# Kernel optimization log

Hardware: AMD Instinct MI355X
Metric: run time of the kernel (lower is better)

The kernel has to match this reference:

```python
import jax, jax.numpy as jnp
import numpy as np

# dims derived from init_kwargs
B, C, T, F = 16, 2, 16, 256
TP, FP = 4, 4            # time/freq patch
MF = F // FP             # 64 freq tokens
TIC = T // TP            # 4 time tokens per chunk
S = MF * TIC             # 256 tokens per chunk
CTX = 3
LEFT = S * CTX           # 768 cached tokens
MT = TIC * (CTX + 1)     # 16 max time positions
D, H, G = 512, 8, 4      # d_model, q heads, kv groups
HD = D // H              # 64
R = H // G               # 2 q-heads per kv group
L = 4                    # layers
FFH = 4 * D
EPS = 1e-5


def _ln(x, g, b):
    m = jnp.mean(x, -1, keepdims=True)
    v = jnp.mean((x - m) ** 2, -1, keepdims=True)
    return (x - m) * jax.lax.rsqrt(v + EPS) * g + b


def setup_inputs() -> dict:
    key = jax.random.key(0)
    ks = iter(jax.random.split(key, 20))
    rn = lambda shape, s=0.05: jax.random.normal(next(ks), shape, jnp.float32) * s
    return {
        "x": rn((B, C, T, F), 1.0),
        "cache_k": rn((L, B, G, LEFT, HD), 1.0),
        "cache_v": rn((L, B, G, LEFT, HD), 1.0),
        "in_W": rn((TP * FP * C, D)), "in_b": jnp.zeros((D,)),
        "ln1_g": jnp.ones((L, D)), "ln1_b": jnp.zeros((L, D)),
        "Wq": rn((L, D, D)), "bq": jnp.zeros((L, D)),
        "Wk": rn((L, D, G * HD)), "bk": jnp.zeros((L, G * HD)),
        "Wv": rn((L, D, G * HD)), "bv": jnp.zeros((L, G * HD)),
        "Wo": rn((L, D, D)), "bo": jnp.zeros((L, D)),
        "rel_time": rn((L, 2 * MT - 1, H)), "rel_freq": rn((L, 2 * MF - 1, H)),
        "res_a": jnp.ones((L,)),
        "ln2_g": jnp.ones((L, D)), "ln2_b": jnp.zeros((L, D)),
        "W1": rn((L, D, FFH)), "b1": jnp.zeros((L, FFH)),
        "W3": rn((L, D, FFH)), "b3": jnp.zeros((L, FFH)),
        "W2": rn((L, FFH, D)), "b2": jnp.zeros((L, D)),
        "res_f": jnp.ones((L,)),
        "out_W": rn((D, TP * FP * C)), "out_b": jnp.zeros((TP * FP * C,)),
    }


def reference(x, cache_k, cache_v, in_W, in_b, ln1_g, ln1_b, Wq, bq, Wk, bk, Wv, bv,
              Wo, bo, rel_time, rel_freq, res_a, ln2_g, ln2_b, W1, b1, W3, b3, W2, b2,
              res_f, out_W, out_b):
    # patchify: (B,C,T,F) -> (B, S, TP*FP*C), token order time-major / freq inner
    h = jnp.transpose(x, (0, 2, 3, 1)).reshape(B, TIC, TP, MF, FP, C)
    h = jnp.transpose(h, (0, 1, 3, 2, 4, 5)).reshape(B, S, TP * FP * C)
    h = h @ in_W + in_b  # (B,S,D)

    # 2D relative position indices (identical each layer)
    K = LEFT + S
    q_idx = jnp.arange(S)
    k_idx = jnp.arange(K)
    qt = LEFT // MF + q_idx // MF  # query time = cache time offset + local time
    qf = q_idx % MF
    kt = k_idx // MF
    kf = k_idx % MF
    dt = qt[:, None] - kt[None, :] + (MT - 1)  # (S,K) in [0, 2*MT-2]
    df = qf[:, None] - kf[None, :] + (MF - 1)  # (S,K) in [0, 2*MF-2]
    scale = 1.0 / np.sqrt(HD).astype(np.float32)

    new_ck, new_cv = [], []
    for l in range(L):
        # --- streaming GQA attention with 2D rel-pos and KV cache ---
        xin = _ln(h, ln1_g[l], ln1_b[l])
        q = (xin @ Wq[l] + bq[l]).reshape(B, S, H, HD)
        k = (xin @ Wk[l] + bk[l]).reshape(B, S, G, HD)
        v = (xin @ Wv[l] + bv[l]).reshape(B, S, G, HD)
        k_full = jnp.concatenate([cache_k[l], jnp.transpose(k, (0, 2, 1, 3))], axis=2)  # (B,G,K,HD)
        v_full = jnp.concatenate([cache_v[l], jnp.transpose(v, (0, 2, 1, 3))], axis=2)
        new_ck.append(k_full[:, :, -LEFT:])
        new_cv.append(v_full[:, :, -LEFT:])
        # group q heads: head h -> group h // R
        scores = jnp.einsum('bsgrd,bgtd->bgrst', q.reshape(B, S, G, R, HD), k_full) * scale
        bias = rel_time[l][dt] + rel_freq[l][df]          # (S,K,H)
        bias = jnp.transpose(bias, (2, 0, 1)).reshape(G, R, S, K)
        attn = jax.nn.softmax(scores + bias[None], axis=-1)
        o = jnp.einsum('bgrst,bgtd->bsgrd', attn, v_full).reshape(B, S, D)
        o = o @ Wo[l] + bo[l]
        h = h + res_a[l] * o  # dropout/droppath identity at eval
        # --- SwiGLU FFN ---
        xin = _ln(h, ln2_g[l], ln2_b[l])
        ff = (jax.nn.silu(xin @ W1[l] + b1[l]) * (xin @ W3[l] + b3[l])) @ W2[l] + b2[l]
        h = h + res_f[l] * ff

    y = h @ out_W + out_b  # (B,S,TP*FP*C)
    # unpatchify back to (B,C,T,F)
    y = y.reshape(B, TIC, MF, TP, FP, C)
    y = jnp.transpose(y, (0, 1, 3, 2, 4, 5)).reshape(B, T, F, C)
    y = jnp.transpose(y, (0, 3, 1, 2))
    return y, jnp.stack(new_ck), jnp.stack(new_cv)
```

## Files before the change

### kernel.cpp

```cpp
#include <hip/hip_runtime.h>
#include <stdint.h>

typedef __attribute__((ext_vector_type(8))) short bf16x8;
typedef __attribute__((ext_vector_type(4))) float f32x4;

#define B_    16
#define S_    256
#define LEFT_ 768
#define KT_   1024
#define D_    512
#define H_    8
#define G_    4
#define HD_   64
#define L_    4
#define FFH_  2048
#define M_    4096

__device__ __forceinline__ unsigned short f2b(float f){
  unsigned u = __float_as_uint(f);
  u += 0x7fffu + ((u>>16)&1u);
  return (unsigned short)(u>>16);
}

__device__ __forceinline__ void gl_lds16(const unsigned short* g, void* l){
  __builtin_amdgcn_global_load_lds(
    (const __attribute__((address_space(1))) unsigned int*)g,
    (__attribute__((address_space(3))) unsigned int*)l, 16, 0, 0);
}

template<int BM, int BN, int WM, int WN, class BRowF>
__device__ __forceinline__ void mfma_core(
    const unsigned short* Abase, int lda, int m0, BRowF brow,
    int kd, char* As, char* Bs, f32x4* acc)
{
  constexpr int FR = WM/16, FC = WN/16;
  constexpr int NWC = BN/WN;
  constexpr int CA = BM/64, CB = BN/64;
  const int tid = threadIdx.x, wave = tid>>6, lane = tid&63;
  const int wr = wave / NWC, wc = wave % NWC;
  const int lr = lane>>2;
  const int swl = (lane&3) ^ ((lane>>2)&3) ^ (lane>>4);

  auto stage = [&](int buf, int k0){
    #pragma unroll
    for (int i = 0; i < CA; ++i) {
      const int chunk = wave*CA + i;
      const unsigned short* gp = Abase + (size_t)(m0 + chunk*16 + lr)*lda + k0 + swl*8;
      gl_lds16(gp, As + buf*(BM*64) + chunk*1024);
    }
    #pragma unroll
    for (int i = 0; i < CB; ++i) {
      const int chunk = wave*CB + i;
      const unsigned short* gp = brow(chunk*16 + lr) + k0 + swl*8;
      gl_lds16(gp, Bs + buf*(BN*64) + chunk*1024);
    }
  };

  stage(0, 0);
  __syncthreads();
  int cur = 0;
  for (int k0 = 0; k0 < kd; k0 += 32) {
    if (k0 + 32 < kd) stage(cur^1, k0 + 32);
    bf16x8 af[FR], bfr[FC];
    #pragma unroll
    for (int r = 0; r < FR; ++r)
      af[r] = *(const bf16x8*)(As + cur*(BM*64) + (wr*WM + r*16 + (lane&15))*64 + swl*16);
    #pragma unroll
    for (int c = 0; c < FC; ++c)
      bfr[c] = *(const bf16x8*)(Bs + cur*(BN*64) + (wc*WN + c*16 + (lane&15))*64 + swl*16);
    #pragma unroll
    for (int r = 0; r < FR; ++r)
      #pragma unroll
      for (int c = 0; c < FC; ++c)
        acc[r*FC+c] = __builtin_amdgcn_mfma_f32_16x16x32_bf16(af[r], bfr[c], acc[r*FC+c], 0, 0, 0);
    __syncthreads();
    cur ^= 1;
  }
}

__device__ __forceinline__ void tcvt_body(
    const float* __restrict__ src, unsigned short* __restrict__ dst,
    int K, int N, int ntk, int ntn, int bx)
{
  __shared__ float t[64][65];
  int kt = bx % ntk; int nt = (bx/ntk) % ntn; int l = bx/(ntk*ntn);
  src += (size_t)l*K*N; dst += (size_t)l*N*K;
  const int k0 = kt*64, n0 = nt*64;
  const int tid = threadIdx.x;
  #pragma unroll
  for (int i = 0; i < 4; ++i) {
    int kr = (tid>>4) + i*16;
    const float4 v = *(const float4*)&src[(size_t)(k0+kr)*N + n0 + (tid&15)*4];
    t[kr][(tid&15)*4+0]=v.x; t[kr][(tid&15)*4+1]=v.y;
    t[kr][(tid&15)*4+2]=v.z; t[kr][(tid&15)*4+3]=v.w;
  }
  __syncthreads();
  const int nn = tid>>2, kk = (tid&3)*16;
  unsigned w[8];
  #pragma unroll
  for (int j = 0; j < 8; ++j)
    w[j] = (unsigned)f2b(t[kk+2*j][nn]) | ((unsigned)f2b(t[kk+2*j+1][nn])<<16);
  size_t off = (size_t)(n0+nn)*K + k0 + kk;
  *(uint4*)&dst[off]     = make_uint4(w[0],w[1],w[2],w[3]);
  *(uint4*)&dst[off + 8] = make_uint4(w[4],w[5],w[6],w[7]);
}

__global__ __launch_bounds__(256) void transpose_all(
    const float* __restrict__ Wq, const float* __restrict__ Wk,
    const float* __restrict__ Wv, const float* __restrict__ Wo,
    const float* __restrict__ W1, const float* __restrict__ W3,
    const float* __restrict__ W2,
    unsigned short* __restrict__ Wqt, unsigned short* __restrict__ Wkt,
    unsigned short* __restrict__ Wvt, unsigned short* __restrict__ Wot,
    unsigned short* __restrict__ W1t, unsigned short* __restrict__ W3t,
    unsigned short* __restrict__ W2t)
{
  int bx = blockIdx.x;
  if      (bx < 256)  tcvt_body(Wq, Wqt, 512, 512, 8, 8,  bx);
  else if (bx < 384)  tcvt_body(Wk, Wkt, 512, 256, 8, 4,  bx-256);
  else if (bx < 512)  tcvt_body(Wv, Wvt, 512, 256, 8, 4,  bx-384);
  else if (bx < 768)  tcvt_body(Wo, Wot, 512, 512, 8, 8,  bx-512);
  else if (bx < 1792) tcvt_body(W1, W1t, 512, 2048, 8, 32, bx-768);
  else if (bx < 2816) tcvt_body(W3, W3t, 512, 2048, 8, 32, bx-1792);
  else                tcvt_body(W2, W2t, 2048, 512, 32, 8, bx-2816);
}

__global__ __launch_bounds__(256) void patchify_inproj(
    const float* __restrict__ x, const float* __restrict__ inW,
    const float* __restrict__ inb, float* __restrict__ h)
{
  int bs = blockIdx.x;
  int b = bs >> 8, s = bs & 255;
  int tic = s >> 6, mf = s & 63;
  __shared__ float ps[32];
  int tid = threadIdx.x;
  if (tid < 32) {
    int tp = tid >> 3, fp = (tid >> 1) & 3, c = tid & 1;
    ps[tid] = x[((size_t)(b*2 + c)*16 + tic*4 + tp)*256 + mf*4 + fp];
  }
  __syncthreads();
  #pragma unroll
  for (int rep = 0; rep < 2; ++rep) {
    int d = tid + rep*256;
    float acc = inb[d];
    #pragma unroll
    for (int i = 0; i < 32; ++i) acc += ps[i] * inW[i*D_ + d];
    h[(size_t)bs*D_ + d] = acc;
  }
}

__global__ __launch_bounds__(256) void ln_kernel(
    const float* __restrict__ in, unsigned short* __restrict__ out,
    const float* __restrict__ g, const float* __restrict__ bta)
{
  size_t row = blockIdx.x;
  const float* rp = in + row*D_;
  int tid = threadIdx.x;
  float x0 = rp[tid], x1 = rp[tid+256];
  float s = x0 + x1, sq = x0*x0 + x1*x1;
  __shared__ float red[10];
  #pragma unroll
  for (int o = 32; o > 0; o >>= 1) {
    s  += __shfl_down(s,  o, 64);
    sq += __shfl_down(sq, o, 64);
  }
  if ((tid & 63) == 0) { red[tid>>6] = s; red[4 + (tid>>6)] = sq; }
  __syncthreads();
  if (tid == 0) {
    float ts = red[0]+red[1]+red[2]+red[3];
    float tq = red[4]+red[5]+red[6]+red[7];
    float mean = ts * (1.0f/D_);
    float var  = tq * (1.0f/D_) - mean*mean;
    red[8] = mean; red[9] = 1.0f / sqrtf(var + 1e-5f);
  }
  __syncthreads();
  float mean = red[8], inv = red[9];
  unsigned short* op = out + row*D_;
  op[tid]     = f2b((x0-mean)*inv*g[tid]     + bta[tid]);
  op[tid+256] = f2b((x1-mean)*inv*g[tid+256] + bta[tid+256]);
}

__global__ __launch_bounds__(256) void qkv_ln_gemm(
    const float* __restrict__ h,
    const float* __restrict__ lng, const float* __restrict__ lnb,
    const unsigned short* __restrict__ Wqt, const unsigned short* __restrict__ Wkt,
    const unsigned short* __restrict__ Wvt,
    const float* __restrict__ bq, const float* __restrict__ bk_, const float* __restrict__ bv_,
    unsigned short* __restrict__ q_bf, unsigned short* __restrict__ kf_bf,
    unsigned short* __restrict__ vt_bf, float* __restrict__ nck, float* __restrict__ ncv)
{
  __shared__ alignas(16) char As[2][64*64];
  __shared__ alignas(16) char Bs[2][128*64];
  __shared__ float sm[64], sr[64];
  const int bx = blockIdx.x;
  const int mt = bx >> 3, nt = bx & 7;
  const int m0 = mt*64, n0 = nt*128;
  const int tid = threadIdx.x, wave = tid>>6, lane = tid&63;

  {
    const int r = tid >> 2, qd = tid & 3;
    const float* rp = h + (size_t)(m0 + r)*512 + qd*128;
    float s = 0.f, sq = 0.f;
    #pragma unroll
    for (int i = 0; i < 32; ++i) {
      float4 v = ((const float4*)rp)[i];
      s  += (v.x+v.y)+(v.z+v.w);
      sq += (v.x*v.x+v.y*v.y)+(v.z*v.z+v.w*v.w);
    }
    s += __shfl_xor(s,1,64); sq += __shfl_xor(sq,1,64);
    s += __shfl_xor(s,2,64); sq += __shfl_xor(sq,2,64);
    if (qd == 0) {
      float mean = s*(1.f/512.f);
      sm[r] = mean;
      sr[r] = rsqrtf(sq*(1.f/512.f) - mean*mean + 1e-5f);
    }
  }

  const int ar = tid >> 2, au = tid & 3;
  const int ap = au ^ (ar&3) ^ ((ar>>2)&3);
  const float* arow = h + (size_t)(m0 + ar)*512;

  const int lr = lane>>2;
  const int swl = (lane&3) ^ ((lane>>2)&3) ^ (lane>>4);
  auto brow = [&](int rr) -> const unsigned short* {
    int n = n0 + rr;
    return n < 512 ? Wqt + (size_t)n*512
         : n < 768 ? Wkt + (size_t)(n-512)*512
                   : Wvt + (size_t)(n-768)*512;
  };
  auto stageB = [&](int buf, int k0){
    #pragma unroll
    for (int i = 0; i < 2; ++i) {
      const int chunk = wave*2 + i;
      gl_lds16(brow(chunk*16+lr) + k0 + swl*8, (char*)Bs[buf] + chunk*1024);
    }
  };

  __syncthreads();
  const float mean_r = sm[ar], rstd_r = sr[ar];

  float4 av[6];
  auto loadA = [&](int k0){
    av[0] = *(const float4*)(arow + k0 + au*8);
    av[1] = *(const float4*)(arow + k0 + au*8 + 4);
    av[2] = *(const float4*)(lng  + k0 + au*8);
    av[3] = *(const float4*)(lng  + k0 + au*8 + 4);
    av[4] = *(const float4*)(lnb  + k0 + au*8);
    av[5] = *(const float4*)(lnb  + k0 + au*8 + 4);
  };
  auto writeA = [&](int buf){
    const float* xv = (const float*)&av[0];
    const float* gv = (const float*)&av[2];
    const float* bv2 = (const float*)&av[4];
    unsigned w[4];
    #pragma unroll
    for (int j = 0; j < 4; ++j) {
      float e0 = (xv[2*j]   - mean_r)*rstd_r*gv[2*j]   + bv2[2*j];
      float e1 = (xv[2*j+1] - mean_r)*rstd_r*gv[2*j+1] + bv2[2*j+1];
      w[j] = (unsigned)f2b(e0) | ((unsigned)f2b(e1)<<16);
    }
    *(uint4*)((char*)As[buf] + ar*64 + ap*16) = make_uint4(w[0],w[1],w[2],w[3]);
  };

  loadA(0);
  stageB(0, 0);
  writeA(0);
  __syncthreads();

  f32x4 acc[8] = {};
  const int wr = wave >> 1, wc = wave & 1;
  for (int k0 = 0; k0 < 512; k0 += 32) {
    const int cur = (k0>>5)&1;
    const bool more = (k0 + 32 < 512);
    if (more) { stageB(cur^1, k0+32); loadA(k0+32); }
    bf16x8 af[2], bfv[4];
    #pragma unroll
    for (int r = 0; r < 2; ++r)
      af[r] = *(const bf16x8*)((char*)As[cur] + (wr*32 + r*16 + (lane&15))*64 + swl*16);
    #pragma unroll
    for (int c = 0; c < 4; ++c)
      bfv[c] = *(const bf16x8*)((char*)Bs[cur] + (wc*64 + c*16 + (lane&15))*64 + swl*16);
    #pragma unroll
    for (int r = 0; r < 2; ++r)
      #pragma unroll
      for (int c = 0; c < 4; ++c)
        acc[r*4+c] = __builtin_amdgcn_mfma_f32_16x16x32_bf16(af[r], bfv[c], acc[r*4+c], 0,0,0);
    if (more) writeA(cur^1);
    __syncthreads();
  }

  #pragma unroll
  for (int r = 0; r < 2; ++r)
  #pragma unroll
  for (int c = 0; c < 4; ++c) {
    f32x4 v = acc[r*4+c];
    #pragma unroll
    for (int reg = 0; reg < 4; ++reg) {
      int m = m0 + wr*32 + r*16 + ((lane>>4)<<2) + reg;
      int n = n0 + wc*64 + c*16 + (lane&15);
      float val = v[reg];
      int b = m >> 8, s = m & 255;
      if (n < 512) {
        q_bf[(size_t)m*512 + n] = f2b(val + bq[n]);
      } else if (n < 768) {
        int g = (n-512) >> 6, hd = n & 63;
        float kv = val + bk_[n-512];
        kf_bf[((size_t)(b*4+g)*1024 + 768 + s)*64 + hd] = f2b(kv);
        nck [((size_t)(b*4+g)*768  + 512 + s)*64 + hd] = kv;
      } else {
        int g = (n-768) >> 6, hd = n & 63;
        float vv = val + bv_[n-768];
        vt_bf[((size_t)(b*4+g)*64 + hd)*1024 + 768 + s] = f2b(vv);
        ncv  [((size_t)(b*4+g)*768 + 512 + s)*64 + hd] = vv;
      }
    }
  }
}

__global__ __launch_bounds__(256) void merge_kv(
    const float* __restrict__ ck, const float* __restrict__ cv,
    unsigned short* __restrict__ kf_bf, unsigned short* __restrict__ vt_bf,
    float* __restrict__ nck, float* __restrict__ ncv)
{
  __shared__ float t[64][65];
  const int bb = blockIdx.x;
  const int tid = threadIdx.x;
  if (bb < 3072) {
    size_t idx = (size_t)bb*256 + tid;
    int hd4 = idx & 15;
    size_t tt = (idx >> 4) % 768;
    size_t bg = idx / (16*768);
    const float4 v = ((const float4*)ck)[idx];
    uint2 pk;
    pk.x = (unsigned)f2b(v.x) | ((unsigned)f2b(v.y)<<16);
    pk.y = (unsigned)f2b(v.z) | ((unsigned)f2b(v.w)<<16);
    *(uint2*)&kf_bf[((bg*1024 + tt)*64) + hd4*4] = pk;
    if (tt >= 256)
      ((float4*)nck)[(bg*768 + (tt-256))*16 + hd4] = v;
  } else {
    const int bi = bb - 3072;
    const int bg = bi / 12, tt = bi % 12;
    const int t0 = tt*64;
    #pragma unroll
    for (int i = 0; i < 4; ++i) {
      int tr = (tid>>4) + i*16;
      const float4 v = ((const float4*)cv)[((size_t)bg*768 + t0+tr)*16 + (tid&15)];
      t[tr][(tid&15)*4+0]=v.x; t[tr][(tid&15)*4+1]=v.y;
      t[tr][(tid&15)*4+2]=v.z; t[tr][(tid&15)*4+3]=v.w;
      if (t0+tr >= 256)
        ((float4*)ncv)[((size_t)bg*768 + t0+tr-256)*16 + (tid&15)] = v;
    }
    __syncthreads();
    const int hd = tid>>2, tc = (tid&3)*16;
    unsigned w[8];
    #pragma unroll
    for (int j = 0; j < 8; ++j)
      w[j] = (unsigned)f2b(t[tc+2*j][hd]) | ((unsigned)f2b(t[tc+2*j+1][hd])<<16);
    size_t off = ((size_t)bg*64 + hd)*1024 + t0 + tc;
    *(uint4*)&vt_bf[off]     = make_uint4(w[0],w[1],w[2],w[3]);
    *(uint4*)&vt_bf[off + 8] = make_uint4(w[4],w[5],w[6],w[7]);
  }
}

__global__ __launch_bounds__(256) void flash_attn(
    const unsigned short* __restrict__ q_bf,
    const unsigned short* __restrict__ kf_bf,
    const unsigned short* __restrict__ vt_bf,
    const float* __restrict__ relt,
    const float* __restrict__ relf,
    unsigned short* __restrict__ att_bf)
{
  const int bx = blockIdx.x;
  const int qt = bx & 3, hh = (bx>>2) & 7, b = bx >> 5;
  const int g = hh >> 1;
  const int tid = threadIdx.x, wave = tid>>6, lane = tid&63;
  const int lg = lane>>4, lq = lane&15;
  const int q0 = qt*64;

  __shared__ alignas(16) char Ks[2][16384];
  __shared__ alignas(16) char Vs[2][16384];

  const unsigned short* kfb  = kf_bf + (size_t)(b*4+g)*1024*64;
  const unsigned short* vtb2 = vt_bf + (size_t)(b*4+g)*64*1024;

  auto stage = [&](int buf, int t){
    #pragma unroll
    for (int it = 0; it < 4; ++it) {
      int slot = it*256 + tid;
      int kr = slot>>3, kp = slot&7,  ku = kp ^ (kr&7);
      gl_lds16(kfb + (size_t)(t*128 + kr)*64 + ku*8, Ks[buf] + slot*16);
      int vr = slot>>4, vp = slot&15, vu = vp ^ (vr&15);
      gl_lds16(vtb2 + (size_t)vr*1024 + t*128 + vu*8, Vs[buf] + slot*16);
    }
  };

  const unsigned short* qrow = q_bf + ((size_t)(b*256 + q0 + wave*16 + lq))*512 + hh*64;
  bf16x8 qfrag[2];
  qfrag[0] = *(const bf16x8*)(qrow + lg*8);
  qfrag[1] = *(const bf16x8*)(qrow + 32 + lg*8);

  float bias_f[4][4];
  {
    int sq = wave*16 + lq;
    #pragma unroll
    for (int f = 0; f < 4; ++f)
      #pragma unroll
      for (int r = 0; r < 4; ++r)
        bias_f[f][r] = relf[((sq - (f*16 + lg*4 + r)) + 63)*8 + hh];
  }

  f32x4 ot[4] = {};
  float m_run = -1e30f, l_part = 0.f;

  stage(0, 0);
  __syncthreads();

  for (int t = 0; t < 8; ++t) {
    const int cur = t & 1;
    if (t + 1 < 8) stage(cur^1, t+1);

    f32x4 st[8] = {};
    #pragma unroll
    for (int c = 0; c < 2; ++c)
      #pragma unroll
      for (int f = 0; f < 8; ++f) {
        int row = f*16 + lq;
        int pu = (c*4 + lg) ^ (row & 7);
        bf16x8 kf_ = *(const bf16x8*)(Ks[cur] + row*128 + pu*16);
        st[f] = __builtin_amdgcn_mfma_f32_16x16x32_bf16(kf_, qfrag[c], st[f], 0,0,0);
      }

    const float bt0 = relt[(27 + qt - 2*t)*8 + hh];
    const float bt1 = relt[(27 + qt - 2*t - 1)*8 + hh];
    float mt = -1e30f;
    #pragma unroll
    for (int f = 0; f < 8; ++f) {
      const float bt = (f < 4) ? bt0 : bt1;
      #pragma unroll
      for (int r = 0; r < 4; ++r) {
        float v = st[f][r]*0.125f + bt + bias_f[f&3][r];
        st[f][r] = v;
        mt = fmaxf(mt, v);
      }
    }
    mt = fmaxf(mt, __shfl_xor(mt, 16, 64));
    mt = fmaxf(mt, __shfl_xor(mt, 32, 64));
    const float m_new = fmaxf(m_run, mt);
    const float corr = __expf(m_run - m_new);
    m_run = m_new;
    l_part *= corr;
    #pragma unroll
    for (int f = 0; f < 4; ++f) {
      ot[f][0] *= corr; ot[f][1] *= corr; ot[f][2] *= corr; ot[f][3] *= corr;
    }
    float psum = 0.f;
    unsigned r01[8], r23[8];
    #pragma unroll
    for (int f = 0; f < 8; ++f) {
      float e0 = __expf(st[f][0] - m_new);
      float e1 = __expf(st[f][1] - m_new);
      float e2 = __expf(st[f][2] - m_new);
      float e3 = __expf(st[f][3] - m_new);
      psum += (e0+e1)+(e2+e3);
      r01[f] = (unsigned)f2b(e0) | ((unsigned)f2b(e1)<<16);
      r23[f] = (unsigned)f2b(e2) | ((unsigned)f2b(e3)<<16);
    }
    l_part += psum;

    const int src0 = (lg&1)*32 + lq;
    const int src1 = src0 + 16;
    const bool hi = (lg>>1) != 0;
    #pragma unroll
    for (int c = 0; c < 4; ++c) {
      unsigned a0 = (unsigned)__shfl((int)r01[c*2],   src0, 64);
      unsigned b0 = (unsigned)__shfl((int)r01[c*2+1], src0, 64);
      unsigned a1 = (unsigned)__shfl((int)r23[c*2],   src0, 64);
      unsigned b1 = (unsigned)__shfl((int)r23[c*2+1], src0, 64);
      unsigned a2 = (unsigned)__shfl((int)r01[c*2],   src1, 64);
      unsigned b2 = (unsigned)__shfl((int)r01[c*2+1], src1, 64);
      unsigned a3 = (unsigned)__shfl((int)r23[c*2],   src1, 64);
      unsigned b3 = (unsigned)__shfl((int)r23[c*2+1], src1, 64);
      uint4 bw;
      bw.x = hi ? b0 : a0;
      bw.y = hi ? b1 : a1;
      bw.z = hi ? b2 : a2;
      bw.w = hi ? b3 : a3;
      bf16x8 pfrag = *(bf16x8*)&bw;
      #pragma unroll
      for (int f = 0; f < 4; ++f) {
        int row = f*16 + lq;
        int pu = (c*4 + lg) ^ (row & 15);
        bf16x8 vf_ = *(const bf16x8*)(Vs[cur] + row*256 + pu*16);
        ot[f] = __builtin_amdgcn_mfma_f32_16x16x32_bf16(vf_, pfrag, ot[f], 0,0,0);
      }
    }
    __syncthreads();
  }

  float l_tot = l_part + __shfl_xor(l_part, 16, 64);
  l_tot += __shfl_xor(l_tot, 32, 64);
  const float inv = 1.0f / l_tot;
  unsigned short* orow = att_bf + ((size_t)(b*256 + q0 + wave*16 + lq))*512 + hh*64;
  #pragma unroll
  for (int f = 0; f < 4; ++f) {
    uint2 w;
    w.x = (unsigned)f2b(ot[f][0]*inv) | ((unsigned)f2b(ot[f][1]*inv)<<16);
    w.y = (unsigned)f2b(ot[f][2]*inv) | ((unsigned)f2b(ot[f][3]*inv)<<16);
    *(uint2*)(orow + f*16 + lg*4) = w;
  }
}

__global__ __launch_bounds__(256) void ffn1_gemm(
    const unsigned short* __restrict__ xin,
    const unsigned short* __restrict__ W1t, const unsigned short* __restrict__ W3t,
    const float* __restrict__ b1_, const float* __restrict__ b3_,
    unsigned short* __restrict__ ff_bf)
{
  __shared__ alignas(16) char As[2*128*64];
  __shared__ alignas(16) char Bs[2*128*64];
  f32x4 acc[16] = {};
  const int bx = blockIdx.x;
  const int nt = bx & 31, mt = bx >> 5;
  const int m0 = mt*128, n0 = nt*128;
  auto brow = [&](int r) -> const unsigned short* {
    int p = n0 + r;
    int pb = p >> 4;
    int j = ((pb>>1)<<4) | (p & 15);
    return (pb & 1) ? W3t + (size_t)j*512 : W1t + (size_t)j*512;
  };
  mfma_core<128,128,64,64>(xin, 512, m0, brow, 512, As, Bs, acc);
  const int lane = threadIdx.x & 63, wave = threadIdx.x >> 6;
  const int wr = wave >> 1, wc = wave & 1;
  #pragma unroll
  for (int r = 0; r < 4; ++r)
  #pragma unroll
  for (int cp = 0; cp < 4; cp += 2) {
    f32x4 va = acc[r*4+cp];
    f32x4 vb = acc[r*4+cp+1];
    #pragma unroll
    for (int reg = 0; reg < 4; ++reg) {
      int m = m0 + wr*64 + r*16 + ((lane>>4)<<2) + reg;
      int p = n0 + wc*64 + cp*16 + (lane&15);
      int j = ((p>>5)<<4) | (p & 15);
      float a = va[reg] + b1_[j];
      float bb = vb[reg] + b3_[j];
      float gval = (a / (1.0f + __expf(-a))) * bb;
      ff_bf[(size_t)m*2048 + j] = f2b(gval);
    }
  }
}

__global__ __launch_bounds__(256) void res_gemm(
    const unsigned short* __restrict__ A, int lda,
    const unsigned short* __restrict__ Wt, int kd,
    const float* __restrict__ bias, const float* __restrict__ resv,
    float* __restrict__ h)
{
  __shared__ alignas(16) char As[2*64*64];
  __shared__ alignas(16) char Bs[2*64*64];
  f32x4 acc[4] = {};
  const int bx = blockIdx.x;
  const int mt = bx >> 3, nt = bx & 7;
  const int m0 = mt*64, n0 = nt*64;
  auto brow = [&](int r) -> const unsigned short* {
    return Wt + (size_t)(n0 + r)*kd;
  };
  mfma_core<64,64,32,32>(A, lda, m0, brow, kd, As, Bs, acc);
  const float rv = resv[0];
  const int lane = threadIdx.x & 63, wave = threadIdx.x >> 6;
  const int wr = wave >> 1, wc = wave & 1;
  #pragma unroll
  for (int r = 0; r < 2; ++r)
  #pragma unroll
  for (int c = 0; c < 2; ++c) {
    f32x4 v = acc[r*2+c];
    #pragma unroll
    for (int reg = 0; reg < 4; ++reg) {
      int m = m0 + wr*32 + r*16 + ((lane>>4)<<2) + reg;
      int n = n0 + wc*32 + c*16 + (lane&15);
      h[(size_t)m*512 + n] += rv * (v[reg] + bias[n]);
    }
  }
}

__global__ __launch_bounds__(256) void outproj_kernel(
    const float* __restrict__ h, const float* __restrict__ outW,
    const float* __restrict__ outb, float* __restrict__ y)
{
  int bs = blockIdx.x;
  int b = bs >> 8, s = bs & 255;
  int tic = s >> 6, mf = s & 63;
  __shared__ float hr[512];
  __shared__ float part[8][32];
  int tid = threadIdx.x;
  hr[tid]     = h[(size_t)bs*D_ + tid];
  hr[tid+256] = h[(size_t)bs*D_ + tid + 256];
  __syncthreads();
  int i = tid & 31, seg = tid >> 5;
  float acc = 0.0f;
  #pragma unroll
  for (int k = 0; k < 64; ++k) acc += hr[seg*64 + k] * outW[(seg*64 + k)*32 + i];
  part[seg][i] = acc;
  __syncthreads();
  if (tid < 32) {
    float v = outb[tid];
    #pragma unroll
    for (int s2 = 0; s2 < 8; ++s2) v += part[s2][tid];
    int tp = tid >> 3, fp = (tid >> 1) & 3, c = tid & 1;
    y[((size_t)(b*2 + c)*16 + tic*4 + tp)*256 + mf*4 + fp] = v;
  }
}

extern "C" void kernel_launch(void* const* d_in, const int* in_sizes, int n_in,
                              void* d_out, int out_size, void* d_ws, size_t ws_size,
                              hipStream_t stream) {
  (void)in_sizes; (void)n_in; (void)out_size; (void)ws_size;
  const float* x        = (const float*)d_in[0];
  const float* cache_k  = (const float*)d_in[1];
  const float* cache_v  = (const float*)d_in[2];
  const float* in_W     = (const float*)d_in[3];
  const float* in_b     = (const float*)d_in[4];
  const float* ln1_g    = (const float*)d_in[5];
  const float* ln1_b    = (const float*)d_in[6];
  const float* Wq       = (const float*)d_in[7];
  const float* bq       = (const float*)d_in[8];
  const float* Wk       = (const float*)d_in[9];
  const float* bk       = (const float*)d_in[10];
  const float* Wv       = (const float*)d_in[11];
  const float* bv       = (const float*)d_in[12];
  const float* Wo       = (const float*)d_in[13];
  const float* bo       = (const float*)d_in[14];
  const float* rel_time = (const float*)d_in[15];
  const float* rel_freq = (const float*)d_in[16];
  const float* res_a    = (const float*)d_in[17];
  const float* ln2_g    = (const float*)d_in[18];
  const float* ln2_b    = (const float*)d_in[19];
  const float* W1       = (const float*)d_in[20];
  const float* b1       = (const float*)d_in[21];
  const float* W3       = (const float*)d_in[22];
  const float* b3       = (const float*)d_in[23];
  const float* W2       = (const float*)d_in[24];
  const float* b2       = (const float*)d_in[25];
  const float* res_f    = (const float*)d_in[26];
  const float* out_W    = (const float*)d_in[27];
  const float* out_b    = (const float*)d_in[28];

  char* ws = (char*)d_ws;
  size_t o = 0;
  float* h            = (float*)(ws + o);          o += (size_t)4096*512*4;
  unsigned short* xin = (unsigned short*)(ws + o); o += (size_t)4096*512*2;
  unsigned short* qb  = (unsigned short*)(ws + o); o += (size_t)4096*512*2;
  unsigned short* att = (unsigned short*)(ws + o); o += (size_t)4096*512*2;
  unsigned short* kfb = (unsigned short*)(ws + o); o += (size_t)64*1024*64*2;
  unsigned short* vtb = (unsigned short*)(ws + o); o += (size_t)64*64*1024*2;
  unsigned short* Wqt = (unsigned short*)(ws + o); o += (size_t)4*512*512*2;
  unsigned short* Wkt = (unsigned short*)(ws + o); o += (size_t)4*256*512*2;
  unsigned short* Wvt = (unsigned short*)(ws + o); o += (size_t)4*256*512*2;
  unsigned short* Wot = (unsigned short*)(ws + o); o += (size_t)4*512*512*2;
  unsigned short* W1t = (unsigned short*)(ws + o); o += (size_t)4*2048*512*2;
  unsigned short* W3t = (unsigned short*)(ws + o); o += (size_t)4*2048*512*2;
  unsigned short* W2t = (unsigned short*)(ws + o); o += (size_t)4*512*2048*2;
  unsigned short* ffb = (unsigned short*)(ws + o);

  float* y    = (float*)d_out;
  float* nck0 = y + 131072;
  float* ncv0 = nck0 + 12582912;

  transpose_all<<<3840, 256, 0, stream>>>(Wq, Wk, Wv, Wo, W1, W3, W2,
                                          Wqt, Wkt, Wvt, Wot, W1t, W3t, W2t);

  patchify_inproj<<<M_, 256, 0, stream>>>(x, in_W, in_b, h);

  for (int l = 0; l < L_; ++l) {
    qkv_ln_gemm<<<512, 256, 0, stream>>>(
        h, ln1_g + l*512, ln1_b + l*512,
        Wqt + (size_t)l*512*512, Wkt + (size_t)l*256*512, Wvt + (size_t)l*256*512,
        bq + l*512, bk + l*256, bv + l*256,
        qb, kfb, vtb, nck0 + (size_t)l*3145728, ncv0 + (size_t)l*3145728);
    merge_kv<<<3840, 256, 0, stream>>>(
        cache_k + (size_t)l*3145728, cache_v + (size_t)l*3145728,
        kfb, vtb, nck0 + (size_t)l*3145728, ncv0 + (size_t)l*3145728);
    flash_attn<<<512, 256, 0, stream>>>(qb, kfb, vtb,
        rel_time + l*31*8, rel_freq + l*127*8, att);
    res_gemm<<<512, 256, 0, stream>>>(att, 512, Wot + (size_t)l*512*512, 512,
                                      bo + l*512, res_a + l, h);
    ln_kernel<<<M_, 256, 0, stream>>>(h, xin, ln2_g + l*512, ln2_b + l*512);
    ffn1_gemm<<<1024, 256, 0, stream>>>(
        xin, W1t + (size_t)l*2048*512, W3t + (size_t)l*2048*512,
        b1 + l*2048, b3 + l*2048, ffb);
    res_gemm<<<512, 256, 0, stream>>>(ffb, 2048, W2t + (size_t)l*512*2048, 2048,
                                      b2 + l*512, res_f + l, h);
  }

  outproj_kernel<<<M_, 256, 0, stream>>>(h, out_W, out_b, y);
}
```

Measured before the change: 690.6 us.

## Stage new V rows contiguously and transpose in merge_kv; skip redundant softmax rescale

```diff
diff --git a/kernel.cpp b/kernel.cpp
--- a/kernel.cpp
+++ b/kernel.cpp
@@ -187,7 +187,7 @@
     const unsigned short* __restrict__ Wvt,
     const float* __restrict__ bq, const float* __restrict__ bk_, const float* __restrict__ bv_,
     unsigned short* __restrict__ q_bf, unsigned short* __restrict__ kf_bf,
-    unsigned short* __restrict__ vt_bf, float* __restrict__ nck, float* __restrict__ ncv)
+    unsigned short* __restrict__ vnew, float* __restrict__ nck, float* __restrict__ ncv)
 {
   __shared__ alignas(16) char As[2][64*64];
   __shared__ alignas(16) char Bs[2][128*64];
@@ -310,8 +310,8 @@
       } else {
         int g = (n-768) >> 6, hd = n & 63;
         float vv = val + bv_[n-768];
-        vt_bf[((size_t)(b*4+g)*64 + hd)*1024 + 768 + s] = f2b(vv);
-        ncv  [((size_t)(b*4+g)*768 + 512 + s)*64 + hd] = vv;
+        vnew[(size_t)m*256 + (n-768)] = f2b(vv);
+        ncv [((size_t)(b*4+g)*768 + 512 + s)*64 + hd] = vv;
       }
     }
   }
@@ -319,6 +319,7 @@
 
 __global__ __launch_bounds__(256) void merge_kv(
     const float* __restrict__ ck, const float* __restrict__ cv,
+    const unsigned short* __restrict__ vnew,
     unsigned short* __restrict__ kf_bf, unsigned short* __restrict__ vt_bf,
     float* __restrict__ nck, float* __restrict__ ncv)
 {
@@ -337,7 +338,7 @@
     *(uint2*)&kf_bf[((bg*1024 + tt)*64) + hd4*4] = pk;
     if (tt >= 256)
       ((float4*)nck)[(bg*768 + (tt-256))*16 + hd4] = v;
-  } else {
+  } else if (bb < 3840) {
     const int bi = bb - 3072;
     const int bg = bi / 12, tt = bi % 12;
     const int t0 = tt*64;
@@ -356,6 +357,31 @@
     #pragma unroll
     for (int j = 0; j < 8; ++j)
       w[j] = (unsigned)f2b(t[tc+2*j][hd]) | ((unsigned)f2b(t[tc+2*j+1][hd])<<16);
+    size_t off = ((size_t)bg*64 + hd)*1024 + t0 + tc;
+    *(uint4*)&vt_bf[off]     = make_uint4(w[0],w[1],w[2],w[3]);
+    *(uint4*)&vt_bf[off + 8] = make_uint4(w[4],w[5],w[6],w[7]);
+  } else {
+    const int bi = bb - 3840;
+    const int bg = bi >> 2, tt4 = bi & 3;
+    const int b = bg >> 2, g = bg & 3;
+    const int t0 = 768 + tt4*64;
+    unsigned short* ts = (unsigned short*)&t[0][0];
+    #pragma unroll
+    for (int i = 0; i < 4; ++i) {
+      int tr = (tid>>4) + i*16;
+      uint2 v = *(const uint2*)&vnew[((size_t)(b*256 + (t0-768) + tr))*256 + g*64 + (tid&15)*4];
+      const unsigned short* pv4 = (const unsigned short*)&v;
+      ts[tr*68 + (tid&15)*4 + 0] = pv4[0];
+      ts[tr*68 + (tid&15)*4 + 1] = pv4[1];
+      ts[tr*68 + (tid&15)*4 + 2] = pv4[2];
+      ts[tr*68 + (tid&15)*4 + 3] = pv4[3];
+    }
+    __syncthreads();
+    const int hd = tid>>2, tc = (tid&3)*16;
+    unsigned w[8];
+    #pragma unroll
+    for (int j = 0; j < 8; ++j)
+      w[j] = (unsigned)ts[(tc+2*j)*68 + hd] | ((unsigned)ts[(tc+2*j+1)*68 + hd] << 16);
     size_t off = ((size_t)bg*64 + hd)*1024 + t0 + tc;
     *(uint4*)&vt_bf[off]     = make_uint4(w[0],w[1],w[2],w[3]);
     *(uint4*)&vt_bf[off + 8] = make_uint4(w[4],w[5],w[6],w[7]);
@@ -445,22 +471,24 @@
     }
     mt = fmaxf(mt, __shfl_xor(mt, 16, 64));
     mt = fmaxf(mt, __shfl_xor(mt, 32, 64));
-    const float m_new = fmaxf(m_run, mt);
-    const float corr = __expf(m_run - m_new);
-    m_run = m_new;
-    l_part *= corr;
-    #pragma unroll
-    for (int f = 0; f < 4; ++f) {
-      ot[f][0] *= corr; ot[f][1] *= corr; ot[f][2] *= corr; ot[f][3] *= corr;
+    if (!__all(mt - m_run <= 8.0f)) {
+      const float m_new = fmaxf(m_run, mt);
+      const float corr = __expf(m_run - m_new);
+      m_run = m_new;
+      l_part *= corr;
+      #pragma unroll
+      for (int f = 0; f < 4; ++f) {
+        ot[f][0] *= corr; ot[f][1] *= corr; ot[f][2] *= corr; ot[f][3] *= corr;
+      }
     }
     float psum = 0.f;
     unsigned r01[8], r23[8];
     #pragma unroll
     for (int f = 0; f < 8; ++f) {
-      float e0 = __expf(st[f][0] - m_new);
-      float e1 = __expf(st[f][1] - m_new);
-      float e2 = __expf(st[f][2] - m_new);
-      float e3 = __expf(st[f][3] - m_new);
+      float e0 = __expf(st[f][0] - m_run);
+      float e1 = __expf(st[f][1] - m_run);
+      float e2 = __expf(st[f][2] - m_run);
+      float e3 = __expf(st[f][3] - m_run);
       psum += (e0+e1)+(e2+e3);
       r01[f] = (unsigned)f2b(e0) | ((unsigned)f2b(e1)<<16);
       r23[f] = (unsigned)f2b(e2) | ((unsigned)f2b(e3)<<16);
@@ -653,6 +681,7 @@
   unsigned short* att = (unsigned short*)(ws + o); o += (size_t)4096*512*2;
   unsigned short* kfb = (unsigned short*)(ws + o); o += (size_t)64*1024*64*2;
   unsigned short* vtb = (unsigned short*)(ws + o); o += (size_t)64*64*1024*2;
+  unsigned short* vnw = (unsigned short*)(ws + o); o += (size_t)4096*256*2;
   unsigned short* Wqt = (unsigned short*)(ws + o); o += (size_t)4*512*512*2;
   unsigned short* Wkt = (unsigned short*)(ws + o); o += (size_t)4*256*512*2;
   unsigned short* Wvt = (unsigned short*)(ws + o); o += (size_t)4*256*512*2;
@@ -676,9 +705,9 @@
         h, ln1_g + l*512, ln1_b + l*512,
         Wqt + (size_t)l*512*512, Wkt + (size_t)l*256*512, Wvt + (size_t)l*256*512,
         bq + l*512, bk + l*256, bv + l*256,
-        qb, kfb, vtb, nck0 + (size_t)l*3145728, ncv0 + (size_t)l*3145728);
-    merge_kv<<<3840, 256, 0, stream>>>(
-        cache_k + (size_t)l*3145728, cache_v + (size_t)l*3145728,
+        qb, kfb, vnw, nck0 + (size_t)l*3145728, ncv0 + (size_t)l*3145728);
+    merge_kv<<<4096, 256, 0, stream>>>(
+        cache_k + (size_t)l*3145728, cache_v + (size_t)l*3145728, vnw,
         kfb, vtb, nck0 + (size_t)l*3145728, ncv0 + (size_t)l*3145728);
     flash_attn<<<512, 256, 0, stream>>>(qb, kfb, vtb,
         rel_time + l*31*8, rel_freq + l*127*8, att);
```

Result: faster. 665.4 us (-3.7%).
